# Kernel tuning notes

Measured on AMD Instinct MI355X. Metric: run time of the kernel, lower is better.

The kernel has to match this reference:

```python
import jax, jax.numpy as jnp
import numpy as np

B, S, D_MODEL, N_HEADS, D_HEAD = 2, 2048, 2048, 16, 128


def _rope_tables(seq_len, d_head, base=10000.0):
    # standard llama RoPE cos/sin tables, broadcastable to (B, H, S, d_head)
    inv_freq = 1.0 / (base ** (np.arange(0, d_head, 2, dtype=np.float32) / d_head))
    t = np.arange(seq_len, dtype=np.float32)
    freqs = np.outer(t, inv_freq)                      # (S, d_head/2)
    emb = np.concatenate([freqs, freqs], axis=-1)       # (S, d_head)
    cos = jnp.asarray(np.cos(emb))[None, None]          # (1,1,S,d_head)
    sin = jnp.asarray(np.sin(emb))[None, None]
    return cos, sin


def setup_inputs() -> dict:
    key = jax.random.key(0)
    ks = jax.random.split(key, 5)
    scale = 0.02
    x = jax.random.normal(ks[0], (B, S, D_MODEL), dtype=jnp.float32)
    Wq = jax.random.normal(ks[1], (D_MODEL, D_MODEL), dtype=jnp.float32) * scale
    Wk = jax.random.normal(ks[2], (D_MODEL, D_MODEL), dtype=jnp.float32) * scale
    Wv = jax.random.normal(ks[3], (D_MODEL, D_MODEL), dtype=jnp.float32) * scale
    Wo = jax.random.normal(ks[4], (D_MODEL, D_MODEL), dtype=jnp.float32) * scale
    cos, sin = _rope_tables(S, D_HEAD)
    return {"x": x, "cos": cos, "sin": sin, "Wq": Wq, "Wk": Wk, "Wv": Wv, "Wo": Wo}


def _rotate_half(x):
    x1, x2 = jnp.split(x, 2, axis=-1)
    return jnp.concatenate([-x2, x1], axis=-1)


def _apply_rope(x, cos, sin):
    return x * cos + _rotate_half(x) * sin


def reference(x, cos, sin, Wq, Wk, Wv, Wo):
    b, s, _ = x.shape
    # QKV projections (nn.Linear computes x @ W.T), reshape to (B, H, S, Dh)
    def proj(W):
        return (x @ W.T).reshape(b, s, N_HEADS, D_HEAD).transpose(0, 2, 1, 3)
    q = _apply_rope(proj(Wq), cos, sin)
    k = _apply_rope(proj(Wk), cos, sin)
    v = proj(Wv)
    # causal scaled dot-product attention
    scale = 1.0 / jnp.sqrt(jnp.asarray(D_HEAD, dtype=x.dtype))
    scores = jnp.einsum("bhqd,bhkd->bhqk", q, k) * scale
    causal = jnp.tril(jnp.ones((s, s), dtype=bool))
    scores = jnp.where(causal, scores, jnp.asarray(-jnp.inf, dtype=scores.dtype))
    attn = jax.nn.softmax(scores, axis=-1)
    vals = jnp.einsum("bhqk,bhkd->bhqd", attn, v)
    vals = vals.transpose(0, 2, 1, 3).reshape(b, s, D_MODEL)
    return vals @ Wo.T
```

## Files before the change

kernel.cpp:

```cpp
#include <hip/hip_runtime.h>

#define S_LEN 2048
#define DMODEL 2048
#define NHEADS 16
#define DHEAD 128
#define BATCH 2

typedef unsigned short u16;
typedef __attribute__((ext_vector_type(8))) __bf16 bf16x8;
typedef __attribute__((ext_vector_type(4))) float f32x4;

__device__ __forceinline__ u16 f2bf(float f) {
    union { float f; unsigned int u; } a; a.f = f;
    unsigned int u = a.u;
    u += 0x7fffu + ((u >> 16) & 1u);
    return (u16)(u >> 16);
}
__device__ __forceinline__ u16 f2bf_fast(float f) {
    union { float f; unsigned int u; } a; a.f = f;
    return (u16)((a.u + 0x8000u) >> 16);
}
__device__ __forceinline__ float bf2f(u16 b) {
    union { unsigned int u; float f; } a; a.u = ((unsigned int)b) << 16;
    return a.f;
}

__device__ __forceinline__ void g2l16(const void* g, void* l) {
    __builtin_amdgcn_global_load_lds((const __attribute__((address_space(1))) unsigned int*)g,
                                     (__attribute__((address_space(3))) unsigned int*)l,
                                     16, 0, 0);
}

__global__ void cvt_all(const float* __restrict__ x,
                        const float* __restrict__ w0, const float* __restrict__ w1,
                        const float* __restrict__ w2, const float* __restrict__ w3,
                        u16* __restrict__ xb, u16* __restrict__ wdst) {
    int y = blockIdx.y;
    const float* src;
    u16* out;
    if (y < 2) {
        src = x + (size_t)y * 4194304;
        out = xb + (size_t)y * 4194304;
    } else {
        src = (y == 2) ? w0 : (y == 3) ? w1 : (y == 4) ? w2 : w3;
        out = wdst + (size_t)(y - 2) * DMODEL * DMODEL;
    }
    int i = blockIdx.x * 256 + threadIdx.x;
    f32x4 v = *(const f32x4*)(src + (size_t)i * 4);
    ushort4 o;
    o.x = f2bf(v[0]); o.y = f2bf(v[1]); o.z = f2bf(v[2]); o.w = f2bf(v[3]);
    *(ushort4*)(out + (size_t)i * 4) = o;
}

#define QK_PRESCALE 0.12751744f
__global__ void rope_kernel(u16* __restrict__ Q, u16* __restrict__ K,
                            const float* __restrict__ cosT, const float* __restrict__ sinT) {
    u16* T = blockIdx.z ? K : Q;
    const float pre = blockIdx.z ? 1.0f : QK_PRESCALE;
    int bh = blockIdx.y;
    int t = blockIdx.x * 256 + threadIdx.x;
    int s = t >> 4;
    int d4 = (t & 15) * 4;
    u16* row = T + ((size_t)bh * S_LEN + s) * DHEAD;
    ushort4 lo = *(ushort4*)&row[d4];
    ushort4 hi = *(ushort4*)&row[d4 + 64];
    f32x4 cv = *(const f32x4*)&cosT[s * DHEAD + d4];
    f32x4 sv = *(const f32x4*)&sinT[s * DHEAD + d4];
    float l0 = bf2f(lo.x), l1 = bf2f(lo.y), l2 = bf2f(lo.z), l3 = bf2f(lo.w);
    float h0 = bf2f(hi.x), h1 = bf2f(hi.y), h2 = bf2f(hi.z), h3 = bf2f(hi.w);
    ushort4 olo, ohi;
    olo.x = f2bf((l0 * cv[0] - h0 * sv[0]) * pre);
    olo.y = f2bf((l1 * cv[1] - h1 * sv[1]) * pre);
    olo.z = f2bf((l2 * cv[2] - h2 * sv[2]) * pre);
    olo.w = f2bf((l3 * cv[3] - h3 * sv[3]) * pre);
    ohi.x = f2bf((h0 * cv[0] + l0 * sv[0]) * pre);
    ohi.y = f2bf((h1 * cv[1] + l1 * sv[1]) * pre);
    ohi.z = f2bf((h2 * cv[2] + l2 * sv[2]) * pre);
    ohi.w = f2bf((h3 * cv[3] + l3 * sv[3]) * pre);
    *(ushort4*)&row[d4]      = olo;
    *(ushort4*)&row[d4 + 64] = ohi;
}

__global__ __launch_bounds__(256) void gemm_qkv(const u16* __restrict__ A,
                                                const u16* __restrict__ W,
                                                u16* __restrict__ Qo,
                                                u16* __restrict__ Ko,
                                                u16* __restrict__ Vto) {
    __shared__ u16 As[128 * 32];
    __shared__ u16 Ws[128 * 32];
    const int tid  = threadIdx.x;
    const int lane = tid & 63;
    const int wave = tid >> 6;
    const int wm = wave >> 1, wn = wave & 1;
    const int col = lane & 15, quad = lane >> 4;
    const int blk = blockIdx.x;
    const int xcd = blk & 7;
    const int loc = blk >> 3;
    const int nb  = xcd * 6 + loc % 6;
    const int mb  = loc / 6;
    const int m0 = mb * 128, n0 = nb * 128;
    const int K = DMODEL;
    const int which = n0 >> 11;

    const u16* P0 = (which == 2) ? A : W;
    const u16* P1 = (which == 2) ? W : A;
    const int  r0 = (which == 2) ? m0 : n0;
    const int  r1 = (which == 2) ? n0 : m0;

    f32x4 acc[4][4] = {};

    const int swl = (quad ^ ((col >> 1) & 3)) * 8;
    int a_off[4], w_off[4];
    #pragma unroll
    for (int mi = 0; mi < 4; ++mi) a_off[mi] = (wm * 64 + mi * 16 + col) * 32 + swl;
    #pragma unroll
    for (int ni = 0; ni < 4; ++ni) w_off[ni] = (wn * 64 + ni * 16 + col) * 32 + swl;

    for (int kk = 0; kk < K; kk += 32) {
        #pragma unroll
        for (int i = 0; i < 2; ++i) {
            int c = i * 256 + tid;
            int row = c >> 2;
            int ko = (((c & 3) ^ ((c >> 3) & 3))) * 8;
            int cb = i * 256 + wave * 64;
            g2l16(P0 + (size_t)(r0 + row) * K + kk + ko, (void*)(As + cb * 8));
            g2l16(P1 + (size_t)(r1 + row) * K + kk + ko, (void*)(Ws + cb * 8));
        }
        __syncthreads();
        bf16x8 af[4], wf[4];
        #pragma unroll
        for (int mi = 0; mi < 4; ++mi) af[mi] = *(const bf16x8*)&As[a_off[mi]];
        #pragma unroll
        for (int ni = 0; ni < 4; ++ni) wf[ni] = *(const bf16x8*)&Ws[w_off[ni]];
        #pragma unroll
        for (int mi = 0; mi < 4; ++mi)
            #pragma unroll
            for (int ni = 0; ni < 4; ++ni)
                acc[mi][ni] = __builtin_amdgcn_mfma_f32_16x16x32_bf16(af[mi], wf[ni], acc[mi][ni], 0, 0, 0);
        __syncthreads();
    }

    if (which == 2) {
        #pragma unroll
        for (int mi = 0; mi < 4; ++mi) {
            #pragma unroll
            for (int ni = 0; ni < 4; ++ni) {
                int s0   = m0 + wm * 64 + mi * 16 + quad * 4;
                int ncol = (n0 & 2047) + wn * 64 + ni * 16 + col;
                int b = s0 >> 11, s = s0 & 2047;
                int h = ncol >> 7, d = ncol & 127;
                ushort4 o;
                o.x = f2bf(acc[mi][ni][0]); o.y = f2bf(acc[mi][ni][1]);
                o.z = f2bf(acc[mi][ni][2]); o.w = f2bf(acc[mi][ni][3]);
                *(ushort4*)&Vto[(((size_t)(b * NHEADS + h)) * DHEAD + d) * S_LEN + s] = o;
            }
        }
    } else {
        u16* out = which ? Ko : Qo;
        #pragma unroll
        for (int mi = 0; mi < 4; ++mi) {
            #pragma unroll
            for (int ni = 0; ni < 4; ++ni) {
                int dd = (n0 & 2047) + wm * 64 + mi * 16 + quad * 4;
                int sg = m0 + wn * 64 + ni * 16 + col;
                int b = sg >> 11, s = sg & 2047;
                int h = dd >> 7, d = dd & 127;
                ushort4 o;
                o.x = f2bf(acc[mi][ni][0]); o.y = f2bf(acc[mi][ni][1]);
                o.z = f2bf(acc[mi][ni][2]); o.w = f2bf(acc[mi][ni][3]);
                *(ushort4*)&out[(((size_t)(b * NHEADS + h)) * S_LEN + s) * DHEAD + d] = o;
            }
        }
    }
}

__global__ __launch_bounds__(256) void gemm_out(const u16* __restrict__ A,
                                                const u16* __restrict__ W,
                                                float* __restrict__ out) {
    __shared__ u16 As[128 * 32];
    __shared__ u16 Ws[128 * 32];
    const int tid  = threadIdx.x;
    const int lane = tid & 63;
    const int wave = tid >> 6;
    const int wm = wave >> 1, wn = wave & 1;
    const int col = lane & 15, quad = lane >> 4;
    const int blk = blockIdx.x;
    const int xcd = blk & 7;
    const int loc = blk >> 3;
    const int nb  = xcd * 2 + (loc & 1);
    const int mb  = loc >> 1;
    const int m0 = mb * 128, n0 = nb * 128;
    const int K = DMODEL;

    f32x4 acc[4][4] = {};

    const int swl = (quad ^ ((col >> 1) & 3)) * 8;
    int a_off[4], w_off[4];
    #pragma unroll
    for (int mi = 0; mi < 4; ++mi) a_off[mi] = (wm * 64 + mi * 16 + col) * 32 + swl;
    #pragma unroll
    for (int ni = 0; ni < 4; ++ni) w_off[ni] = (wn * 64 + ni * 16 + col) * 32 + swl;

    for (int kk = 0; kk < K; kk += 32) {
        #pragma unroll
        for (int i = 0; i < 2; ++i) {
            int c = i * 256 + tid;
            int row = c >> 2;
            int ko = (((c & 3) ^ ((c >> 3) & 3))) * 8;
            int cb = i * 256 + wave * 64;
            g2l16(A + (size_t)(m0 + row) * K + kk + ko, (void*)(As + cb * 8));
            g2l16(W + (size_t)(n0 + row) * K + kk + ko, (void*)(Ws + cb * 8));
        }
        __syncthreads();
        bf16x8 af[4], wf[4];
        #pragma unroll
        for (int mi = 0; mi < 4; ++mi) af[mi] = *(const bf16x8*)&As[a_off[mi]];
        #pragma unroll
        for (int ni = 0; ni < 4; ++ni) wf[ni] = *(const bf16x8*)&Ws[w_off[ni]];
        #pragma unroll
        for (int mi = 0; mi < 4; ++mi)
            #pragma unroll
            for (int ni = 0; ni < 4; ++ni)
                acc[mi][ni] = __builtin_amdgcn_mfma_f32_16x16x32_bf16(af[mi], wf[ni], acc[mi][ni], 0, 0, 0);
        __syncthreads();
    }

    #pragma unroll
    for (int mi = 0; mi < 4; ++mi)
        #pragma unroll
        for (int ni = 0; ni < 4; ++ni)
            #pragma unroll
            for (int r = 0; r < 4; ++r) {
                int row  = m0 + wm * 64 + mi * 16 + quad * 4 + r;
                int ncol = n0 + wn * 64 + ni * 16 + col;
                out[(size_t)row * DMODEL + ncol] = acc[mi][ni][r];
            }
}

__global__ __launch_bounds__(512, 4) void attn_kernel(const u16* __restrict__ Q,
                                                      const u16* __restrict__ K,
                                                      const u16* __restrict__ Vt,
                                                      u16* __restrict__ Ao) {
    __shared__ u16 Ks[32 * 136];
    __shared__ u16 Vs[128 * 40];
    __shared__ u16 Ps[8][16 * 40];

    const int tid  = threadIdx.x;
    const int lane = tid & 63;
    const int wave = tid >> 6;
    const int col = lane & 15, quad = lane >> 4;
    const int xcd = blockIdx.x & 7;
    const int sub = (blockIdx.x >> 3) & 3;
    const int bh  = xcd * 4 + sub;
    const int qtile = 15 - (int)(blockIdx.x >> 5);
    const int b = bh >> 4, h = bh & 15;
    const int qb = qtile * 128;
    const int qw = qb + wave * 16;

    const u16* Qb = Q  + (size_t)bh * S_LEN * DHEAD;
    const u16* Kb = K  + (size_t)bh * S_LEN * DHEAD;
    const u16* Vb = Vt + (size_t)bh * DHEAD * S_LEN;

    bf16x8 qf[4];
    #pragma unroll
    for (int dc = 0; dc < 4; ++dc)
        qf[dc] = *(const bf16x8*)&Qb[(size_t)(qw + col) * DHEAD + dc * 32 + quad * 8];

    f32x4 accO[8] = {};
    float lrow = 0.0f;

    const int kr = tid >> 4, ko = (tid & 15) * 8;
    const int vr = tid >> 2, vo = (tid & 3) * 8;

    f32x4 kA = *(const f32x4*)&Kb[(size_t)kr * DHEAD + ko];
    f32x4 vA = *(const f32x4*)&Vb[(size_t)vr * S_LEN + vo];

    const int kend = qb + 128;
    for (int kb = 0; kb < kend; kb += 32) {
        *(f32x4*)&Ks[kr * 136 + ko] = kA;
        *(f32x4*)&Vs[vr * 40 + vo] = vA;
        __syncthreads();

        const int kn = kb + 32;
        if (kn < kend) {
            kA = *(const f32x4*)&Kb[(size_t)(kn + kr) * DHEAD + ko];
            vA = *(const f32x4*)&Vb[(size_t)vr * S_LEN + kn + vo];
        }

        if (kb <= qw + 15) {
            f32x4 sc[2] = {};
            #pragma unroll
            for (int t = 0; t < 2; ++t)
                #pragma unroll
                for (int dc = 0; dc < 4; ++dc) {
                    bf16x8 kf = *(const bf16x8*)&Ks[(t * 16 + col) * 136 + dc * 32 + quad * 8];
                    sc[t] = __builtin_amdgcn_mfma_f32_16x16x32_bf16(kf, qf[dc], sc[t], 0, 0, 0);
                }

            const int q_g = qw + col;
            float p[2][4];
            #pragma unroll
            for (int t = 0; t < 2; ++t)
                #pragma unroll
                for (int r = 0; r < 4; ++r) {
                    int k_g = kb + t * 16 + quad * 4 + r;
                    float e = exp2f(sc[t][r]);
                    p[t][r] = (k_g <= q_g) ? e : 0.0f;
                    lrow += p[t][r];
                }

            u16* P = Ps[wave];
            #pragma unroll
            for (int t = 0; t < 2; ++t) {
                ushort4 o;
                o.x = f2bf_fast(p[t][0]); o.y = f2bf_fast(p[t][1]);
                o.z = f2bf_fast(p[t][2]); o.w = f2bf_fast(p[t][3]);
                *(ushort4*)&P[col * 40 + t * 16 + quad * 4] = o;
            }
            asm volatile("s_waitcnt lgkmcnt(0)" ::: "memory");
            bf16x8 pf = *(const bf16x8*)&P[col * 40 + quad * 8];

            #pragma unroll
            for (int ni = 0; ni < 8; ++ni) {
                bf16x8 vf = *(const bf16x8*)&Vs[(ni * 16 + col) * 40 + quad * 8];
                accO[ni] = __builtin_amdgcn_mfma_f32_16x16x32_bf16(pf, vf, accO[ni], 0, 0, 0);
            }
        }
        __syncthreads();
    }

    lrow += __shfl_xor(lrow, 16);
    lrow += __shfl_xor(lrow, 32);
    float lb[4];
    #pragma unroll
    for (int r = 0; r < 4; ++r)
        lb[r] = 1.0f / __shfl(lrow, quad * 4 + r);
    #pragma unroll
    for (int ni = 0; ni < 8; ++ni)
        #pragma unroll
        for (int r = 0; r < 4; ++r) {
            int q_g = qw + quad * 4 + r;
            int d = ni * 16 + col;
            Ao[((size_t)(b * S_LEN + q_g)) * DMODEL + h * DHEAD + d] = f2bf(accO[ni][r] * lb[r]);
        }
}

extern "C" void kernel_launch(void* const* d_in, const int* in_sizes, int n_in,
                              void* d_out, int out_size, void* d_ws, size_t ws_size,
                              hipStream_t stream) {
    const float* x    = (const float*)d_in[0];
    const float* cosT = (const float*)d_in[1];
    const float* sinT = (const float*)d_in[2];
    const float* Wq   = (const float*)d_in[3];
    const float* Wk   = (const float*)d_in[4];
    const float* Wv   = (const float*)d_in[5];
    const float* Wo   = (const float*)d_in[6];

    char* ws = (char*)d_ws;
    size_t off = 0;
    auto carve = [&](size_t bytes) {
        void* p = ws + off;
        off += (bytes + 255) & ~(size_t)255;
        return p;
    };
    const size_t xN = (size_t)BATCH * S_LEN * DMODEL;
    const size_t wN = (size_t)DMODEL * DMODEL;
    u16* xb   = (u16*)carve(xN * 2);
    u16* wqkv = (u16*)carve(wN * 2 * 4);
    u16* wob  = wqkv + wN * 3;
    u16* Qb   = (u16*)carve(xN * 2);
    u16* Kb   = (u16*)carve(xN * 2);
    u16* Vtb  = (u16*)carve(xN * 2);
    u16* attn = xb;

    cvt_all<<<dim3(4096, 6), 256, 0, stream>>>(x, Wq, Wk, Wv, Wo, xb, wqkv);

    gemm_qkv<<<dim3(1536), 256, 0, stream>>>(xb, wqkv, Qb, Kb, Vtb);

    rope_kernel<<<dim3(S_LEN * 16 / 256, BATCH * NHEADS, 2), 256, 0, stream>>>(Qb, Kb, cosT, sinT);

    attn_kernel<<<dim3(512), 512, 0, stream>>>(Qb, Kb, Vtb, attn);

    gemm_out<<<dim3(512), 256, 0, stream>>>(attn, wob, (float*)d_out);
}
```

Before: 403.8 us.

## Shrink attention query tile to 64 rows and widen key block to 64

The attention kernel now uses 256-thread blocks with 64 query rows each (1024 blocks instead of 512), and stages 64 keys per iteration instead of 32, processing them as two 32-key sub-blocks. The larger key block halves the number of barrier and global-load rounds per block. The smaller query tile gives finer causal load balancing and more blocks. The trade-off is more shared memory per block and more K/V global reads overall, since each key tile is reloaded by twice as many query tiles.

```diff
diff --git a/kernel.cpp b/kernel.cpp
--- a/kernel.cpp
+++ b/kernel.cpp
@@ -237,13 +237,13 @@
             }
 }
 
-__global__ __launch_bounds__(512, 4) void attn_kernel(const u16* __restrict__ Q,
-                                                      const u16* __restrict__ K,
-                                                      const u16* __restrict__ Vt,
-                                                      u16* __restrict__ Ao) {
-    __shared__ u16 Ks[32 * 136];
-    __shared__ u16 Vs[128 * 40];
-    __shared__ u16 Ps[8][16 * 40];
+__global__ __launch_bounds__(256) void attn_kernel(const u16* __restrict__ Q,
+                                                   const u16* __restrict__ K,
+                                                   const u16* __restrict__ Vt,
+                                                   u16* __restrict__ Ao) {
+    __shared__ u16 Ks[64 * 136];
+    __shared__ u16 Vs[128 * 72];
+    __shared__ u16 Ps[4][16 * 40];
 
     const int tid  = threadIdx.x;
     const int lane = tid & 63;
@@ -252,9 +252,9 @@
     const int xcd = blockIdx.x & 7;
     const int sub = (blockIdx.x >> 3) & 3;
     const int bh  = xcd * 4 + sub;
-    const int qtile = 15 - (int)(blockIdx.x >> 5);
+    const int qtile = 31 - (int)(blockIdx.x >> 5);
     const int b = bh >> 4, h = bh & 15;
-    const int qb = qtile * 128;
+    const int qb = qtile * 64;
     const int qw = qb + wave * 16;
 
     const u16* Qb = Q  + (size_t)bh * S_LEN * DHEAD;
@@ -269,61 +269,80 @@
     f32x4 accO[8] = {};
     float lrow = 0.0f;
 
-    const int kr = tid >> 4, ko = (tid & 15) * 8;
-    const int vr = tid >> 2, vo = (tid & 3) * 8;
-
-    f32x4 kA = *(const f32x4*)&Kb[(size_t)kr * DHEAD + ko];
-    f32x4 vA = *(const f32x4*)&Vb[(size_t)vr * S_LEN + vo];
-
-    const int kend = qb + 128;
-    for (int kb = 0; kb < kend; kb += 32) {
-        *(f32x4*)&Ks[kr * 136 + ko] = kA;
-        *(f32x4*)&Vs[vr * 40 + vo] = vA;
-        __syncthreads();
-
-        const int kn = kb + 32;
+    int krr[4], koo[4], vrr[4], voo[4];
+    #pragma unroll
+    for (int i = 0; i < 4; ++i) {
+        int vid = i * 256 + tid;
+        krr[i] = vid >> 4; koo[i] = (vid & 15) * 8;
+        vrr[i] = vid >> 3; voo[i] = (vid & 7) * 8;
+    }
+
+    f32x4 kv[4], vv[4];
+    #pragma unroll
+    for (int i = 0; i < 4; ++i) {
+        kv[i] = *(const f32x4*)&Kb[(size_t)krr[i] * DHEAD + koo[i]];
+        vv[i] = *(const f32x4*)&Vb[(size_t)vrr[i] * S_LEN + voo[i]];
+    }
+
+    const int kend = qb + 64;
+    for (int kb = 0; kb < kend; kb += 64) {
+        #pragma unroll
+        for (int i = 0; i < 4; ++i) {
+            *(f32x4*)&Ks[krr[i] * 136 + koo[i]] = kv[i];
+            *(f32x4*)&Vs[vrr[i] * 72 + voo[i]] = vv[i];
+        }
+        __syncthreads();
+
+        const int kn = kb + 64;
         if (kn < kend) {
-            kA = *(const f32x4*)&Kb[(size_t)(kn + kr) * DHEAD + ko];
-            vA = *(const f32x4*)&Vb[(size_t)vr * S_LEN + kn + vo];
-        }
-
-        if (kb <= qw + 15) {
-            f32x4 sc[2] = {};
-            #pragma unroll
-            for (int t = 0; t < 2; ++t)
+            #pragma unroll
+            for (int i = 0; i < 4; ++i) {
+                kv[i] = *(const f32x4*)&Kb[(size_t)(kn + krr[i]) * DHEAD + koo[i]];
+                vv[i] = *(const f32x4*)&Vb[(size_t)vrr[i] * S_LEN + kn + voo[i]];
+            }
+        }
+
+        #pragma unroll
+        for (int sb = 0; sb < 2; ++sb) {
+            const int kbs = kb + sb * 32;
+            if (kbs <= qw + 15) {
+                f32x4 sc[2] = {};
                 #pragma unroll
-                for (int dc = 0; dc < 4; ++dc) {
-                    bf16x8 kf = *(const bf16x8*)&Ks[(t * 16 + col) * 136 + dc * 32 + quad * 8];
-                    sc[t] = __builtin_amdgcn_mfma_f32_16x16x32_bf16(kf, qf[dc], sc[t], 0, 0, 0);
+                for (int t = 0; t < 2; ++t)
+                    #pragma unroll
+                    for (int dc = 0; dc < 4; ++dc) {
+                        bf16x8 kf = *(const bf16x8*)&Ks[(sb * 32 + t * 16 + col) * 136 + dc * 32 + quad * 8];
+                        sc[t] = __builtin_amdgcn_mfma_f32_16x16x32_bf16(kf, qf[dc], sc[t], 0, 0, 0);
+                    }
+
+                const int q_g = qw + col;
+                float p[2][4];
+                #pragma unroll
+                for (int t = 0; t < 2; ++t)
+                    #pragma unroll
+                    for (int r = 0; r < 4; ++r) {
+                        int k_g = kbs + t * 16 + quad * 4 + r;
+                        float e = exp2f(sc[t][r]);
+                        p[t][r] = (k_g <= q_g) ? e : 0.0f;
+                        lrow += p[t][r];
+                    }
+
+                u16* P = Ps[wave];
+                #pragma unroll
+                for (int t = 0; t < 2; ++t) {
+                    ushort4 o;
+                    o.x = f2bf_fast(p[t][0]); o.y = f2bf_fast(p[t][1]);
+                    o.z = f2bf_fast(p[t][2]); o.w = f2bf_fast(p[t][3]);
+                    *(ushort4*)&P[col * 40 + t * 16 + quad * 4] = o;
                 }
-
-            const int q_g = qw + col;
-            float p[2][4];
-            #pragma unroll
-            for (int t = 0; t < 2; ++t)
+                asm volatile("s_waitcnt lgkmcnt(0)" ::: "memory");
+                bf16x8 pf = *(const bf16x8*)&P[col * 40 + quad * 8];
+
                 #pragma unroll
-                for (int r = 0; r < 4; ++r) {
-                    int k_g = kb + t * 16 + quad * 4 + r;
-                    float e = exp2f(sc[t][r]);
-                    p[t][r] = (k_g <= q_g) ? e : 0.0f;
-                    lrow += p[t][r];
+                for (int ni = 0; ni < 8; ++ni) {
+                    bf16x8 vf = *(const bf16x8*)&Vs[(ni * 16 + col) * 72 + sb * 32 + quad * 8];
+                    accO[ni] = __builtin_amdgcn_mfma_f32_16x16x32_bf16(pf, vf, accO[ni], 0, 0, 0);
                 }
-
-            u16* P = Ps[wave];
-            #pragma unroll
-            for (int t = 0; t < 2; ++t) {
-                ushort4 o;
-                o.x = f2bf_fast(p[t][0]); o.y = f2bf_fast(p[t][1]);
-                o.z = f2bf_fast(p[t][2]); o.w = f2bf_fast(p[t][3]);
-                *(ushort4*)&P[col * 40 + t * 16 + quad * 4] = o;
-            }
-            asm volatile("s_waitcnt lgkmcnt(0)" ::: "memory");
-            bf16x8 pf = *(const bf16x8*)&P[col * 40 + quad * 8];
-
-            #pragma unroll
-            for (int ni = 0; ni < 8; ++ni) {
-                bf16x8 vf = *(const bf16x8*)&Vs[(ni * 16 + col) * 40 + quad * 8];
-                accO[ni] = __builtin_amdgcn_mfma_f32_16x16x32_bf16(pf, vf, accO[ni], 0, 0, 0);
             }
         }
         __syncthreads();
@@ -379,7 +398,7 @@
 
     rope_kernel<<<dim3(S_LEN * 16 / 256, BATCH * NHEADS, 2), 256, 0, stream>>>(Qb, Kb, cosT, sinT);
 
-    attn_kernel<<<dim3(512), 512, 0, stream>>>(Qb, Kb, Vtb, attn);
+    attn_kernel<<<dim3(1024), 256, 0, stream>>>(Qb, Kb, Vtb, attn);
 
     gemm_out<<<dim3(512), 256, 0, stream>>>(attn, wob, (float*)d_out);
 }
```

New measurement: 388.6 us (median of 2 runs). 1.04x faster.
